# Optimization experiments

Measured on AMD Instinct MI355X. Metric: run time of the kernel, lower is better.

## Reference

```python
import jax, jax.numpy as jnp
import numpy as np

B, IN_DIM, HID, N, ORDER = 128, 2, 64, 1024, 2
NUM_SUPPORTS = 2
IN_TOT = (IN_DIM + HID) * (ORDER * NUM_SUPPORTS + 1)  # 66*5 = 330


def setup_inputs() -> dict:
    key = jax.random.key(0)
    ks = jax.random.split(key, 6)
    inputs = jax.random.normal(ks[0], (B, IN_DIM, N), jnp.float32)
    hx = jax.random.normal(ks[1], (B, HID, N), jnp.float32)
    # row-stochastic-ish diffusion supports, scaled for numerical sanity
    A0 = jax.random.uniform(ks[2], (N, N), jnp.float32) * (2.0 / N)
    A1 = jax.random.uniform(ks[3], (N, N), jnp.float32) * (2.0 / N)
    # 1x1 Conv1d weights (squeezed kernel dim): (out_ch, in_ch)
    W_ru = jax.random.normal(ks[4], (2 * HID, IN_TOT), jnp.float32) * 0.05
    b_ru = jnp.ones((2 * HID,), jnp.float32)  # bias_start=1.0
    W_C = jax.random.normal(ks[5], (HID, IN_TOT), jnp.float32) * 0.05
    b_C = jnp.zeros((HID,), jnp.float32)  # bias_start=0.0
    return {"inputs": inputs, "hx": hx, "A0": A0, "A1": A1,
            "W_ru": W_ru, "b_ru": b_ru, "W_C": W_C, "b_C": b_C}


def _gcn(x, A, order):
    # Chebyshev-like diffusion recursion; x: (B, F, N), A: (N, N)
    x0 = x
    x1 = jnp.einsum('bfn,mn->bfm', x0, A)
    out = [x1]
    for _ in range(2, order + 1):
        x2 = 2.0 * jnp.einsum('bfn,mn->bfm', x1, A) - x0
        out.append(x2)
        x1, x0 = x2, x1
    return jnp.concatenate(out, axis=-2)  # (B, F*order, N)


def _multi_adj_gnn(x, adjs, W, b, order):
    # concat identity + per-support diffusion stacks, then 1x1 conv over channels
    h = jnp.concatenate([x] + [_gcn(x, A, order) for A in adjs], axis=-2)
    return jnp.einsum('bcn,oc->bon', h, W) + b[None, :, None]


def reference(inputs, hx, A0, A1, W_ru, b_ru, W_C, b_C):
    adjs = (A0, A1)
    x = jnp.concatenate([inputs, hx], axis=-2)            # (B, IN+HID, N)
    ru = jax.nn.sigmoid(_multi_adj_gnn(x, adjs, W_ru, b_ru, ORDER))
    r, u = ru[:, :HID, :], ru[:, HID:, :]
    xc = jnp.concatenate([inputs, r * hx], axis=-2)
    Cc = jnp.tanh(_multi_adj_gnn(xc, adjs, W_C, b_C, ORDER))
    return u * hx + (1.0 - u) * Cc                        # (B, HID, N)
```

## Files before the change

kernel.cpp:

```cpp
#include <hip/hip_runtime.h>

using u16 = unsigned short;
using u32 = unsigned int;
typedef __attribute__((ext_vector_type(8))) __bf16 bf16x8;
typedef __attribute__((ext_vector_type(8))) u16 u16x8;
typedef __attribute__((ext_vector_type(4))) float f32x4;

#define DEVI __device__ __forceinline__

constexpr int BN_ = 128;
constexpr int NN  = 1024;
constexpr int CH  = 66;
constexpr int HD  = 64;
constexpr int RR  = BN_ * CH;
constexpr long RN = (long)RR * NN;
constexpr int KTRUE = 330, KPAD = 352;
constexpr long M2 = (long)NN * NN;

DEVI float bf2f(u16 u) { u32 i = ((u32)u) << 16; float f; __builtin_memcpy(&f, &i, 4); return f; }
DEVI u16 f2bf(float f) { u32 i; __builtin_memcpy(&i, &f, 4); i += 0x7fffu + ((i >> 16) & 1u); return (u16)(i >> 16); }

DEVI void gl_lds16(const void* g, void* l) {
  __builtin_amdgcn_global_load_lds((const __attribute__((address_space(1))) u32*)g,
                                   (__attribute__((address_space(3))) u32*)l, 16, 0, 0);
}

template<int TMZ, bool SQ>
__global__ __launch_bounds__(256, 2)
void gemm_db(const u16* __restrict__ Xb, long xzs,
             const u16* __restrict__ Ab, long azs,
             u16* __restrict__ Yb, long ozs)
{
  __shared__ u16 L[3 * 8192];
  const int bid = blockIdx.x;
  const int wg  = (bid & 7) * (gridDim.x >> 3) + (bid >> 3);
  const int z   = wg / TMZ;
  const int rem = wg - z * TMZ;
  const int tm  = rem >> 3, tn = rem & 7;

  const u16* X = Xb + (long)z * xzs;
  const u16* A = Ab + (long)z * azs;
  u16*       Y = Yb + (long)z * ozs;
  const int tid = threadIdx.x, wv = tid >> 6, ln = tid & 63;

  const int r0  = wv * 16 + (ln >> 2);
  const int kch = (((ln & 3) ^ ((r0 >> 1) & 3))) * 8;
  const u16* gX = X + (long)(tm * 128 + r0) * NN + kch;
  const u16* gA = A + (long)(tn * 128 + r0) * NN + kch;
  const int lofs = wv * 512;

  const int frow = ln & 15;
  const int fk   = ((ln >> 4) ^ ((ln >> 1) & 3)) * 8;
  const int wr = wv >> 1, wc = wv & 1;

  f32x4 acc[4][4] = {};

#define STAGE(T, BUF) do {                                  \
    u16* bx_ = &L[(BUF) * 8192 + lofs];                     \
    u16* bb_ = &L[(BUF) * 8192 + 4096 + lofs];              \
    const int k0_ = (T) * 32;                               \
    gl_lds16(gX + k0_,           bx_);                      \
    gl_lds16(gX + k0_ + 64 * NN, bx_ + 2048);               \
    gl_lds16(gA + k0_,           bb_);                      \
    gl_lds16(gA + k0_ + 64 * NN, bb_ + 2048);               \
  } while (0)

  STAGE(0, 0);
  STAGE(1, 1);
  asm volatile("s_waitcnt vmcnt(4)" ::: "memory");
  __builtin_amdgcn_s_barrier();
  __builtin_amdgcn_sched_barrier(0);

  int cur = 0;
  for (int t = 0; t < 32; ++t) {
    const int nx = (cur >= 1) ? cur - 1 : cur + 2;
    if (t + 2 < 32) STAGE(t + 2, nx);
    const u16* bx = &L[cur * 8192];
    const u16* bb = bx + 4096;
    bf16x8 af[4], bfv[4];
#pragma unroll
    for (int m = 0; m < 4; m++) af[m]  = *(const bf16x8*)&bx[(wr * 64 + m * 16 + frow) * 32 + fk];
#pragma unroll
    for (int n = 0; n < 4; n++) bfv[n] = *(const bf16x8*)&bb[(wc * 64 + n * 16 + frow) * 32 + fk];
#pragma unroll
    for (int m = 0; m < 4; m++)
#pragma unroll
      for (int n = 0; n < 4; n++)
        acc[m][n] = __builtin_amdgcn_mfma_f32_16x16x32_bf16(af[m], bfv[n], acc[m][n], 0, 0, 0);
    if (t < 31) {
      if (t + 2 < 32) asm volatile("s_waitcnt vmcnt(4)" ::: "memory");
      else            asm volatile("s_waitcnt vmcnt(0)" ::: "memory");
      __builtin_amdgcn_s_barrier();
      __builtin_amdgcn_sched_barrier(0);
    }
    cur = (cur >= 2) ? 0 : cur + 1;
  }
#undef STAGE

  const int colb = tn * 128 + wc * 64 + frow;
  const int rowb = tm * 128 + wr * 64 + (ln >> 4) * 4;
#pragma unroll
  for (int m = 0; m < 4; m++)
#pragma unroll
    for (int n = 0; n < 4; n++) {
      const int col = colb + n * 16;
#pragma unroll
      for (int q = 0; q < 4; q++) {
        const long r = rowb + m * 16 + q;
        float v = acc[m][n][q];
        if (SQ) v = 2.0f * v - (r == col ? 1.0f : 0.0f);
        Y[r * NN + col] = f2bf(v);
      }
    }
}

template<int O, bool FINAL>
__global__ __launch_bounds__(512)
void proj_f(const u16* __restrict__ part0, const u16* __restrict__ Yb,
            const u16* __restrict__ W, const float* __restrict__ bias,
            const float* __restrict__ hx, const u16* __restrict__ zpad,
            u16* __restrict__ xcrow, float* __restrict__ ubuf,
            float* __restrict__ outp)
{
  __shared__ u16 LB[23040];
  __shared__ u16 LA[5632];
  const int b = blockIdx.y, n0 = blockIdx.x * 64;
  const int tid = threadIdx.x, wv = tid >> 6, ln = tid & 63;

  const int of  = (O == 128) ? wv : (wv >> 1);
  const int nfb = (O == 128) ? 0  : 2 * (wv & 1);
  constexpr int NF = (O == 128) ? 4 : 2;
  const int frow = ln & 15, klane = ln >> 4;

  const u16* wb = W + (long)(of * 16 + frow) * KPAD + klane * 8;
  bf16x8 wf[11];
#pragma unroll
  for (int t = 0; t < 11; ++t) wf[t] = *(const bf16x8*)(wb + t * 32);

  for (int hf = 0; hf < 2; ++hf)
#pragma unroll 1
    for (int ch = 0; ch < 2; ++ch) {
#pragma unroll
      for (int ii = 0; ii < 2; ++ii) {
        const int i = ii * 8 + wv;
        if (i < 11) {
          const int c = ch * 176 + 16 * i + (ln >> 2);
          const u16* src;
          if (c < KTRUE) {
            const int p = c / 66, f = c - 66 * p;
            const u16* base = (p == 0) ? part0 : (Yb + (long)(p - 1) * RN);
            src = base + (long)(b * CH + f) * NN + n0 + hf * 32 + (ln & 3) * 8;
          } else {
            src = zpad;
          }
          gl_lds16(src, (char*)LA + i * 1024);
        }
      }
      __syncthreads();
#pragma unroll
      for (int it = 0; it < 2; ++it) {
        const int q = it * 512 + tid;
        if (q < 704) {
          const int n = q & 31, cch = q >> 5;
          u16x8 v;
#pragma unroll
          for (int j = 0; j < 8; ++j) v[j] = LA[(cch * 8 + j) * 32 + n];
          *(u16x8*)((char*)LB + (hf * 32 + n) * 720 + ch * 352 + cch * 16) = v;
        }
      }
      __syncthreads();
    }

  f32x4 acc[NF] = {};
#pragma unroll
  for (int t = 0; t < 11; ++t) {
#pragma unroll
    for (int j = 0; j < NF; ++j) {
      const int nf = nfb + j;
      const bf16x8 bt = *(const bf16x8*)((char*)LB + (nf * 16 + frow) * 720 + t * 64 + klane * 16);
      acc[j] = __builtin_amdgcn_mfma_f32_16x16x32_bf16(wf[t], bt, acc[j], 0, 0, 0);
    }
  }

  const int orow = klane * 4;
#pragma unroll
  for (int j = 0; j < NF; ++j) {
    const int nf = nfb + j;
    const int ncol = n0 + nf * 16 + frow;
#pragma unroll
    for (int q = 0; q < 4; ++q) {
      const int o = of * 16 + orow + q;
      const float pre = acc[j][q] + bias[o];
      if (!FINAL) {
        const float sg = 1.0f / (1.0f + __expf(-pre));
        if (o < HD) {
          const float hv = hx[(long)(b * HD + o) * NN + ncol];
          xcrow[(long)(b * CH + 2 + o) * NN + ncol] = f2bf(sg * hv);
        } else {
          ubuf[(long)(b * HD + (o - HD)) * NN + ncol] = sg;
        }
      } else {
        const float e  = __expf(2.0f * pre);
        const float cc = 1.0f - 2.0f / (e + 1.0f);
        const long oi = (long)(b * HD + o) * NN + ncol;
        const float u = ubuf[oi];
        outp[oi] = u * hx[oi] + (1.0f - u) * cc;
      }
    }
  }
}

__global__ void build_x(const float* __restrict__ inp, const float* __restrict__ hx,
                        u16* __restrict__ X, u16* __restrict__ XC)
{
  const int row = blockIdx.x;
  const int b = row / 66, f = row - b * 66;
  const int n0 = threadIdx.x * 4;
  const float* s = (f < 2) ? (inp + (long)(b * 2 + f) * NN) : (hx + (long)(b * HD + f - 2) * NN);
  const float4 v = *(const float4*)(s + n0);
  ushort4 o;
  o.x = f2bf(v.x); o.y = f2bf(v.y); o.z = f2bf(v.z); o.w = f2bf(v.w);
  *(ushort4*)&X[(long)row * NN + n0] = o;
  if (f < 2) *(ushort4*)&XC[(long)row * NN + n0] = o;
}

__global__ void xposeA(const float* __restrict__ A0, const float* __restrict__ A1,
                       u16* __restrict__ AT)
{
  __shared__ float Ls[64][65];
  const int z = blockIdx.z;
  const float* A = z ? A1 : A0;
  u16* out = AT + (long)z * M2;
  const int m0 = blockIdx.y * 64, n0 = blockIdx.x * 64;
  const int t = threadIdx.x;
  const int rr = t >> 6, cc = t & 63;
#pragma unroll
  for (int i = 0; i < 16; i++)
    Ls[i * 4 + rr][cc] = A[(long)(m0 + i * 4 + rr) * NN + n0 + cc];
  __syncthreads();
  const int n = t >> 2, mc = (t & 3) * 16;
  u16 tmp[16];
#pragma unroll
  for (int k = 0; k < 16; k++) tmp[k] = f2bf(Ls[mc + k][n]);
  u16* dst = &out[(long)(n0 + n) * NN + m0 + mc];
  *(ushort4*)(dst + 0)  = *(ushort4*)&tmp[0];
  *(ushort4*)(dst + 4)  = *(ushort4*)&tmp[4];
  *(ushort4*)(dst + 8)  = *(ushort4*)&tmp[8];
  *(ushort4*)(dst + 12) = *(ushort4*)&tmp[12];
}

__global__ void prep(const float* __restrict__ A0, const float* __restrict__ A1,
                     const float* __restrict__ Wru, const float* __restrict__ WC,
                     u16* __restrict__ Abf2, u16* __restrict__ Wrub, u16* __restrict__ WCb)
{
  const int gid = blockIdx.x * 256 + threadIdx.x;
  if (gid < 524288) {
    const bool sec = gid >= 262144;
    const float* s = sec ? (A1 + (long)(gid - 262144) * 4) : (A0 + (long)gid * 4);
    u16* d = sec ? (Abf2 + 2 * M2 + (long)(gid - 262144) * 4) : (Abf2 + (long)gid * 4);
    const float4 v = *(const float4*)s;
    ushort4 o; o.x = f2bf(v.x); o.y = f2bf(v.y); o.z = f2bf(v.z); o.w = f2bf(v.w);
    *(ushort4*)d = o;
  } else if (gid < 524288 + 128 * KPAD) {
    const int g = gid - 524288;
    const int o = g / KPAD, c = g - o * KPAD;
    Wrub[g] = f2bf(c < KTRUE ? Wru[o * KTRUE + c] : 0.0f);
  } else if (gid < 524288 + 128 * KPAD + 64 * KPAD) {
    const int g = gid - 524288 - 128 * KPAD;
    const int o = g / KPAD, c = g - o * KPAD;
    WCb[g] = f2bf(c < KTRUE ? WC[o * KTRUE + c] : 0.0f);
  }
}

extern "C" void kernel_launch(void* const* d_in, const int* in_sizes, int n_in,
                              void* d_out, int out_size, void* d_ws, size_t ws_size,
                              hipStream_t stream)
{
  const float* inp = (const float*)d_in[0];
  const float* hx  = (const float*)d_in[1];
  const float* A0  = (const float*)d_in[2];
  const float* A1  = (const float*)d_in[3];
  const float* Wru = (const float*)d_in[4];
  const float* bru = (const float*)d_in[5];
  const float* WC  = (const float*)d_in[6];
  const float* bC  = (const float*)d_in[7];
  float* out = (float*)d_out;

  char* ws = (char*)d_ws;
  u16* Abf2 = (u16*)(ws);
  u16* ATbf = (u16*)(ws + 8388608);
  u16* Wrub = (u16*)(ws + 12582912);
  u16* WCb  = (u16*)(ws + 12673024);
  u16* zpad = (u16*)(ws + 12718080);
  u16* X    = (u16*)(ws + 12718336);
  u16* XC   = (u16*)(ws + 30019840);
  u16* Yb   = (u16*)(ws + 47321344);
  float* ub = out;

  hipMemsetAsync(zpad, 0, 256, stream);
  prep<<<2312, 256, 0, stream>>>(A0, A1, Wru, WC, Abf2, Wrub, WCb);
  xposeA<<<dim3(16, 16, 2), 256, 0, stream>>>(A0, A1, ATbf);
  build_x<<<RR, 256, 0, stream>>>(inp, hx, X, XC);

  gemm_db<64, true><<<128, 256, 0, stream>>>(Abf2, 2 * M2, ATbf, M2, Abf2 + M2, 2 * M2);

  const dim3 gx(16, BN_);
  gemm_db<528, false><<<2112, 256, 0, stream>>>(X, 0, Abf2, M2, Yb, RN);
  proj_f<128, false><<<gx, 512, 0, stream>>>(X, Yb, Wrub, bru, hx, zpad, XC, ub, nullptr);

  gemm_db<528, false><<<2112, 256, 0, stream>>>(XC, 0, Abf2, M2, Yb, RN);
  proj_f<64, true><<<gx, 512, 0, stream>>>(XC, Yb, WCb, bC, hx, zpad, nullptr, ub, out);
}
```

Baseline: 373.4 us.

## Deepen GEMM pipeline to four stages and add 64x64-tile kernel for A^2

The main diffusion GEMM now uses four LDS buffers with three tiles prefetched ahead instead of two, aiming to hide more global-load latency. The small A*A squaring GEMM, which launched only 128 blocks with 128x128 tiles, is moved to a separate kernel with 64x64 tiles and 512 blocks so that more CUs are occupied. LDS per block rises to 64KB for the main GEMM, which may reduce how many blocks fit per CU.

```diff
diff --git a/kernel.cpp b/kernel.cpp
--- a/kernel.cpp
+++ b/kernel.cpp
@@ -25,13 +25,13 @@
                                    (__attribute__((address_space(3))) u32*)l, 16, 0, 0);
 }
 
-template<int TMZ, bool SQ>
+template<int TMZ>
 __global__ __launch_bounds__(256, 2)
 void gemm_db(const u16* __restrict__ Xb, long xzs,
              const u16* __restrict__ Ab, long azs,
              u16* __restrict__ Yb, long ozs)
 {
-  __shared__ u16 L[3 * 8192];
+  __shared__ u16 L[4 * 8192];
   const int bid = blockIdx.x;
   const int wg  = (bid & 7) * (gridDim.x >> 3) + (bid >> 3);
   const int z   = wg / TMZ;
@@ -67,49 +67,131 @@
 
   STAGE(0, 0);
   STAGE(1, 1);
-  asm volatile("s_waitcnt vmcnt(4)" ::: "memory");
+  STAGE(2, 2);
+  asm volatile("s_waitcnt vmcnt(8)" ::: "memory");
+  __builtin_amdgcn_s_barrier();
+  __builtin_amdgcn_sched_barrier(0);
+
+  int cur = 0;
+  for (int t = 0; t < 32; ++t) {
+    if (t + 3 < 32) STAGE(t + 3, (cur + 3) & 3);
+    const u16* bx = &L[cur * 8192];
+    const u16* bb = bx + 4096;
+    bf16x8 af[4], bfv[4];
+#pragma unroll
+    for (int m = 0; m < 4; m++) af[m]  = *(const bf16x8*)&bx[(wr * 64 + m * 16 + frow) * 32 + fk];
+#pragma unroll
+    for (int n = 0; n < 4; n++) bfv[n] = *(const bf16x8*)&bb[(wc * 64 + n * 16 + frow) * 32 + fk];
+#pragma unroll
+    for (int m = 0; m < 4; m++)
+#pragma unroll
+      for (int n = 0; n < 4; n++)
+        acc[m][n] = __builtin_amdgcn_mfma_f32_16x16x32_bf16(af[m], bfv[n], acc[m][n], 0, 0, 0);
+    if (t < 31) {
+      if (t + 3 < 32)   asm volatile("s_waitcnt vmcnt(8)" ::: "memory");
+      else if (t == 29) asm volatile("s_waitcnt vmcnt(4)" ::: "memory");
+      else              asm volatile("s_waitcnt vmcnt(0)" ::: "memory");
+      __builtin_amdgcn_s_barrier();
+      __builtin_amdgcn_sched_barrier(0);
+    }
+    cur = (cur + 1) & 3;
+  }
+#undef STAGE
+
+  const int colb = tn * 128 + wc * 64 + frow;
+  const int rowb = tm * 128 + wr * 64 + (ln >> 4) * 4;
+#pragma unroll
+  for (int m = 0; m < 4; m++)
+#pragma unroll
+    for (int n = 0; n < 4; n++) {
+      const int col = colb + n * 16;
+#pragma unroll
+      for (int q = 0; q < 4; q++) {
+        const long r = rowb + m * 16 + q;
+        Y[r * NN + col] = f2bf(acc[m][n][q]);
+      }
+    }
+}
+
+__global__ __launch_bounds__(256, 2)
+void gemm_sq64(const u16* __restrict__ Xb, long xzs,
+               const u16* __restrict__ Ab, long azs,
+               u16* __restrict__ Yb, long ozs)
+{
+  __shared__ u16 L[3 * 4096];
+  const int bid = blockIdx.x;
+  const int wg  = (bid & 7) * 64 + (bid >> 3);
+  const int z   = wg >> 8;
+  const int rem = wg & 255;
+  const int tm  = rem >> 4, tn = rem & 15;
+
+  const u16* X = Xb + (long)z * xzs;
+  const u16* A = Ab + (long)z * azs;
+  u16*       Y = Yb + (long)z * ozs;
+  const int tid = threadIdx.x, wv = tid >> 6, ln = tid & 63;
+
+  const int r0  = wv * 16 + (ln >> 2);
+  const int kch = (((ln & 3) ^ ((r0 >> 1) & 3))) * 8;
+  const u16* gX = X + (long)(tm * 64 + r0) * NN + kch;
+  const u16* gA = A + (long)(tn * 64 + r0) * NN + kch;
+  const int lofs = wv * 512;
+
+  const int frow = ln & 15;
+  const int fk   = ((ln >> 4) ^ ((ln >> 1) & 3)) * 8;
+  const int wr = wv >> 1, wc = wv & 1;
+
+  f32x4 acc[2][2] = {};
+
+#define STAGE2(T, BUF) do {                                 \
+    const int k0_ = (T) * 32;                               \
+    gl_lds16(gX + k0_, &L[(BUF) * 4096 + lofs]);            \
+    gl_lds16(gA + k0_, &L[(BUF) * 4096 + 2048 + lofs]);     \
+  } while (0)
+
+  STAGE2(0, 0);
+  STAGE2(1, 1);
+  asm volatile("s_waitcnt vmcnt(2)" ::: "memory");
   __builtin_amdgcn_s_barrier();
   __builtin_amdgcn_sched_barrier(0);
 
   int cur = 0;
   for (int t = 0; t < 32; ++t) {
     const int nx = (cur >= 1) ? cur - 1 : cur + 2;
-    if (t + 2 < 32) STAGE(t + 2, nx);
-    const u16* bx = &L[cur * 8192];
-    const u16* bb = bx + 4096;
-    bf16x8 af[4], bfv[4];
-#pragma unroll
-    for (int m = 0; m < 4; m++) af[m]  = *(const bf16x8*)&bx[(wr * 64 + m * 16 + frow) * 32 + fk];
-#pragma unroll
-    for (int n = 0; n < 4; n++) bfv[n] = *(const bf16x8*)&bb[(wc * 64 + n * 16 + frow) * 32 + fk];
-#pragma unroll
-    for (int m = 0; m < 4; m++)
-#pragma unroll
-      for (int n = 0; n < 4; n++)
+    if (t + 2 < 32) STAGE2(t + 2, nx);
+    const u16* bx = &L[cur * 4096];
+    const u16* bb = bx + 2048;
+    bf16x8 af[2], bfv[2];
+#pragma unroll
+    for (int m = 0; m < 2; m++) af[m]  = *(const bf16x8*)&bx[(wr * 32 + m * 16 + frow) * 32 + fk];
+#pragma unroll
+    for (int n = 0; n < 2; n++) bfv[n] = *(const bf16x8*)&bb[(wc * 32 + n * 16 + frow) * 32 + fk];
+#pragma unroll
+    for (int m = 0; m < 2; m++)
+#pragma unroll
+      for (int n = 0; n < 2; n++)
         acc[m][n] = __builtin_amdgcn_mfma_f32_16x16x32_bf16(af[m], bfv[n], acc[m][n], 0, 0, 0);
     if (t < 31) {
-      if (t + 2 < 32) asm volatile("s_waitcnt vmcnt(4)" ::: "memory");
+      if (t + 2 < 32) asm volatile("s_waitcnt vmcnt(2)" ::: "memory");
       else            asm volatile("s_waitcnt vmcnt(0)" ::: "memory");
       __builtin_amdgcn_s_barrier();
       __builtin_amdgcn_sched_barrier(0);
     }
     cur = (cur >= 2) ? 0 : cur + 1;
   }
-#undef STAGE
-
-  const int colb = tn * 128 + wc * 64 + frow;
-  const int rowb = tm * 128 + wr * 64 + (ln >> 4) * 4;
-#pragma unroll
-  for (int m = 0; m < 4; m++)
-#pragma unroll
-    for (int n = 0; n < 4; n++) {
+#undef STAGE2
+
+  const int colb = tn * 64 + wc * 32 + frow;
+  const int rowb = tm * 64 + wr * 32 + (ln >> 4) * 4;
+#pragma unroll
+  for (int m = 0; m < 2; m++)
+#pragma unroll
+    for (int n = 0; n < 2; n++) {
       const int col = colb + n * 16;
 #pragma unroll
       for (int q = 0; q < 4; q++) {
-        const long r = rowb + m * 16 + q;
-        float v = acc[m][n][q];
-        if (SQ) v = 2.0f * v - (r == col ? 1.0f : 0.0f);
-        Y[r * NN + col] = f2bf(v);
+        const int r = rowb + m * 16 + q;
+        const float v = 2.0f * acc[m][n][q] - (r == col ? 1.0f : 0.0f);
+        Y[(long)r * NN + col] = f2bf(v);
       }
     }
 }
@@ -302,12 +384,12 @@
   xposeA<<<dim3(16, 16, 2), 256, 0, stream>>>(A0, A1, ATbf);
   build_x<<<RR, 256, 0, stream>>>(inp, hx, X, XC);
 
-  gemm_db<64, true><<<128, 256, 0, stream>>>(Abf2, 2 * M2, ATbf, M2, Abf2 + M2, 2 * M2);
+  gemm_sq64<<<512, 256, 0, stream>>>(Abf2, 2 * M2, ATbf, M2, Abf2 + M2, 2 * M2);
 
   const dim3 gx(16, BN_);
-  gemm_db<528, false><<<2112, 256, 0, stream>>>(X, 0, Abf2, M2, Yb, RN);
+  gemm_db<528><<<2112, 256, 0, stream>>>(X, 0, Abf2, M2, Yb, RN);
   proj_f<128, false><<<gx, 512, 0, stream>>>(X, Yb, Wrub, bru, hx, zpad, XC, ub, nullptr);
 
-  gemm_db<528, false><<<2112, 256, 0, stream>>>(XC, 0, Abf2, M2, Yb, RN);
+  gemm_db<528><<<2112, 256, 0, stream>>>(XC, 0, Abf2, M2, Yb, RN);
   proj_f<64, true><<<gx, 512, 0, stream>>>(XC, Yb, WCb, bC, hx, zpad, nullptr, ub, out);
 }
```

Result: no change. 377.2 us (+1.0%).
